# Kernel tuning notes

Measured on AMD Instinct MI355X. Metric: run time of the kernel, lower is better.

The kernel has to match this reference:

```python
import jax, jax.numpy as jnp
import numpy as np

C_IN = 128
C_HID = 128


def setup_inputs() -> dict:
    key = jax.random.key(0)
    ks = jax.random.split(key, 10)
    B, I, J = 1, 384, 384
    x = jax.random.normal(ks[0], (B, I, J, C_IN), dtype=jnp.float32)
    mask = jnp.ones((B, I, J), dtype=jnp.float32)
    # LayerNorm params
    ln_gamma = jnp.ones((C_IN,), jnp.float32)
    ln_beta = jnp.zeros((C_IN,), jnp.float32)
    # Projections (stored as [in, out] for x @ W)
    W_a_p = jax.random.normal(ks[1], (C_IN, C_HID), jnp.float32) * 0.02
    b_a_p = jnp.zeros((C_HID,), jnp.float32)
    W_a_g = jax.random.normal(ks[2], (C_IN, C_HID), jnp.float32) * 0.01
    W_b_p = jax.random.normal(ks[3], (C_IN, C_HID), jnp.float32) * 0.02
    b_b_p = jnp.zeros((C_HID,), jnp.float32)
    W_b_g = jax.random.normal(ks[4], (C_IN, C_HID), jnp.float32) * 0.01
    W_z = jax.random.normal(ks[5], (C_HID, C_IN), jnp.float32) * (0.02 / np.sqrt(C_HID))
    b_z = jnp.zeros((C_IN,), jnp.float32)
    return dict(x=x, mask=mask, ln_gamma=ln_gamma, ln_beta=ln_beta,
                W_a_p=W_a_p, b_a_p=b_a_p, W_a_g=W_a_g,
                W_b_p=W_b_p, b_b_p=b_b_p, W_b_g=W_b_g,
                W_z=W_z, b_z=b_z)


def _layer_norm(x, gamma, beta, eps=1e-5):
    mu = jnp.mean(x, axis=-1, keepdims=True)
    var = jnp.mean(jnp.square(x - mu), axis=-1, keepdims=True)
    return (x - mu) * jax.lax.rsqrt(var + eps) * gamma + beta


def reference(x, mask, ln_gamma, ln_beta, W_a_p, b_a_p, W_a_g, W_b_p, b_b_p, W_b_g, W_z, b_z):
    # x: [B, I, J, C_in], mask: [B, I, J]; outgoing triangle multiplication
    xn = _layer_norm(x, ln_gamma, ln_beta)
    m = mask[..., None]
    a = (xn @ W_a_p + b_a_p) * jax.nn.sigmoid(xn @ W_a_g) * m  # [B,I,J,Ch]
    b = (xn @ W_b_p + b_b_p) * jax.nn.sigmoid(xn @ W_b_g) * m  # [B,I,J,Ch]
    # outgoing: sum over k of a[...,i,k,c] * b[...,k,j,c]
    o = jnp.einsum('bikc,bkjc->bijc', a, b)
    o = o @ W_z + b_z
    return x + o
```

## Files before the change

### kernel.cpp

```cpp
#include <hip/hip_runtime.h>

typedef __bf16 bf16;
typedef bf16 bf16x4 __attribute__((ext_vector_type(4)));
typedef bf16 bf16x8 __attribute__((ext_vector_type(8)));
typedef float f32x4 __attribute__((ext_vector_type(4)));
typedef int ivec4 __attribute__((ext_vector_type(4)));

#define PTOT 147456
#define N384 384

static __device__ __forceinline__ f32x4 mfma16(bf16x8 a, bf16x8 b, f32x4 c) {
  return __builtin_amdgcn_mfma_f32_16x16x32_bf16(a, b, c, 0, 0, 0);
}

static __device__ __forceinline__ void gload_lds16(const bf16* g, bf16* lds) {
  __builtin_amdgcn_global_load_lds(
      (const __attribute__((address_space(1))) void*)g,
      (__attribute__((address_space(3))) void*)lds, 16, 0, 0);
}

__global__ __launch_bounds__(256) void k_prep(
    const float* __restrict__ w0, const float* __restrict__ w1,
    const float* __restrict__ w2, const float* __restrict__ w3,
    const float* __restrict__ w4, bf16* __restrict__ wt)
{
  const int m = blockIdx.x;
  const float* src = (m == 0) ? w0 : (m == 1) ? w1 : (m == 2) ? w2 : (m == 3) ? w3 : w4;
  bf16* dst = wt + m * 16384;
  for (int slot = threadIdx.x; slot < 2048; slot += 256) {
    const int l  = slot & 63;
    const int ks = (slot >> 6) & 3;
    const int n  = slot >> 8;
    const int ch = n * 16 + (l & 15);
    const int kb = ks * 32 + (l >> 4) * 8;
    bf16 tmp[8] __attribute__((aligned(16)));
    #pragma unroll
    for (int e = 0; e < 8; ++e)
      tmp[e] = (bf16)src[(size_t)(kb + e) * 128 + ch];
    *(ivec4*)(dst + slot * 8) = *(const ivec4*)tmp;
  }
}

__global__ __launch_bounds__(256) void k1_ln_proj(
    const float* __restrict__ x, const float* __restrict__ mask,
    const float* __restrict__ gamma, const float* __restrict__ beta,
    const float* __restrict__ bap, const float* __restrict__ bbp,
    const bf16* __restrict__ wt,
    bf16* __restrict__ a_t, bf16* __restrict__ b_t)
{
  __shared__ __align__(16) bf16 xn[64 * 128];
  __shared__ __align__(16) bf16 wl[4 * 2 * 4 * 512];
  __shared__ float ml[64];

  const int t = threadIdx.x;
  const int l = t & 63;
  const int w = t >> 6;
  const int p0 = blockIdx.x << 6;
  const int fr = l & 15, fq = l >> 4;

  const bf16* wsrc = wt + w * 16384 + l * 8;
  bf16* wdst = wl + w * 4096;
  #pragma unroll
  for (int n2 = 0; n2 < 2; ++n2)
    #pragma unroll
    for (int ks = 0; ks < 4; ++ks)
      gload_lds16(wsrc + ((n2 * 4 + ks) << 9), wdst + n2 * 2048 + ks * 512);

  if (t < 64) ml[t] = mask[p0 + t];

  const int csub = (t & 7) << 4;
  f32x4 g4[4], bt4[4];
  #pragma unroll
  for (int i = 0; i < 4; ++i) {
    g4[i]  = *(const f32x4*)(gamma + csub + i * 4);
    bt4[i] = *(const f32x4*)(beta  + csub + i * 4);
  }
  #pragma unroll
  for (int it = 0; it < 2; ++it) {
    const int row = (t >> 3) + it * 32;
    f32x4 v[4];
    const float* xb = x + (size_t)(p0 + row) * 128 + csub;
    #pragma unroll
    for (int i = 0; i < 4; ++i) v[i] = *(const f32x4*)(xb + i * 4);

    float s = 0.f, s2 = 0.f;
    #pragma unroll
    for (int i = 0; i < 4; ++i)
      #pragma unroll
      for (int j = 0; j < 4; ++j) { const float f = v[i][j]; s += f; s2 += f * f; }
    #pragma unroll
    for (int m = 1; m < 8; m <<= 1) {
      s  += __shfl_xor(s, m, 64);
      s2 += __shfl_xor(s2, m, 64);
    }
    const float mu = s * (1.f / 128.f);
    const float rs = rsqrtf(s2 * (1.f / 128.f) - mu * mu + 1e-5f);

    bf16x8 xv0, xv1;
    #pragma unroll
    for (int i = 0; i < 4; ++i)
      #pragma unroll
      for (int j = 0; j < 4; ++j) {
        const float f = (v[i][j] - mu) * rs * g4[i][j] + bt4[i][j];
        const int e = i * 4 + j;
        if (e < 8) xv0[e] = (bf16)f; else xv1[e - 8] = (bf16)f;
      }
    const int sw = (row & 7) << 3;
    *(bf16x8*)&xn[row * 128 + (csub ^ sw)]       = xv0;
    *(bf16x8*)&xn[row * 128 + ((csub + 8) ^ sw)] = xv1;
  }
  __syncthreads();

  const int pair = w >> 1;
  const int prow0 = (w & 1) * 32;
  bf16x8 af[2][4];
  #pragma unroll
  for (int mi = 0; mi < 2; ++mi)
    #pragma unroll
    for (int ks = 0; ks < 4; ++ks) {
      const int row = prow0 + mi * 16 + fr;
      af[mi][ks] = *(const bf16x8*)&xn[row * 128 + (((ks * 32 + fq * 8)) ^ ((fr & 7) << 3))];
    }

  const float* bp = pair ? bbp : bap;
  bf16* dst = pair ? b_t : a_t;
  const bf16* wpl = wl + (pair * 2) * 4096 + l * 8;
  const bf16* wgl = wl + (pair * 2 + 1) * 4096 + l * 8;

  #pragma unroll
  for (int p = 0; p < 4; ++p) {
    #pragma unroll
    for (int n2 = 0; n2 < 2; ++n2) {
      const int ch = (p * 2 + n2) * 16 + fr;
      f32x4 aG0 = (f32x4){0.f, 0.f, 0.f, 0.f};
      f32x4 aG1 = (f32x4){0.f, 0.f, 0.f, 0.f};
      #pragma unroll
      for (int ks = 0; ks < 4; ++ks) {
        const bf16x8 bv = *(const bf16x8*)(wgl + n2 * 2048 + ks * 512);
        aG0 = mfma16(af[0][ks], bv, aG0);
        aG1 = mfma16(af[1][ks], bv, aG1);
      }
      f32x4 aP0 = (f32x4){0.f, 0.f, 0.f, 0.f};
      f32x4 aP1 = (f32x4){0.f, 0.f, 0.f, 0.f};
      #pragma unroll
      for (int ks = 0; ks < 4; ++ks) {
        const bf16x8 bv = *(const bf16x8*)(wpl + n2 * 2048 + ks * 512);
        aP0 = mfma16(af[0][ks], bv, aP0);
        aP1 = mfma16(af[1][ks], bv, aP1);
      }
      const float bias = bp[ch];
      #pragma unroll
      for (int mi = 0; mi < 2; ++mi) {
        const f32x4 aG = mi ? aG1 : aG0;
        const f32x4 aP = mi ? aP1 : aP0;
        const int pb = prow0 + mi * 16 + fq * 4;
        const f32x4 m4 = *(const f32x4*)&ml[pb];
        bf16x4 pk;
        #pragma unroll
        for (int r = 0; r < 4; ++r) {
          const float sg = 1.f / (1.f + __expf(-aG[r]));
          pk[r] = (bf16)((aP[r] + bias) * sg * m4[r]);
        }
        *(bf16x4*)(dst + (size_t)ch * PTOT + p0 + pb) = pk;
      }
    }
    if (p < 3) {
      __syncthreads();
      #pragma unroll
      for (int n2 = 0; n2 < 2; ++n2)
        #pragma unroll
        for (int ks = 0; ks < 4; ++ks)
          gload_lds16(wsrc + ((((p + 1) * 2 + n2) * 4 + ks) << 9),
                      wdst + n2 * 2048 + ks * 512);
      __syncthreads();
    }
  }
}

__global__ __launch_bounds__(256) void k2_tri(
    const bf16* __restrict__ a_t, const bf16* __restrict__ b_t, bf16* __restrict__ o_t)
{
  __shared__ __align__(16) bf16 As[128][40];
  __shared__ __align__(16) bf16 Bt[128][40];
  const int t = threadIdx.x, l = t & 63, w = t >> 6;
  const int fr = l & 15, fq = l >> 4;
  const int ti = blockIdx.x;
  const int c  = blockIdx.y;
  const int i0 = (ti / 3) * 128, j0 = (ti % 3) * 128;
  const bf16* ap = a_t + (size_t)c * PTOT;
  const bf16* bp = b_t + (size_t)c * PTOT;
  const int wm = (w >> 1) * 64, wn = (w & 1) * 64;
  const int arow = t >> 2, aseg = t & 3;
  const int bj = t & 127, bkh = (t >> 7) * 16;

  f32x4 acc[4][4];
  #pragma unroll
  for (int mi = 0; mi < 4; ++mi)
    #pragma unroll
    for (int ni = 0; ni < 4; ++ni) acc[mi][ni] = (f32x4){0.f, 0.f, 0.f, 0.f};

  for (int kt = 0; kt < 12; ++kt) {
    const int k0 = kt * 32;
    __syncthreads();
    #pragma unroll
    for (int rep = 0; rep < 2; ++rep) {
      const int row = arow + rep * 64;
      *(ivec4*)&As[row][aseg * 8] =
          *(const ivec4*)(ap + (size_t)(i0 + row) * N384 + k0 + aseg * 8);
    }
    bf16 rb[16] __attribute__((aligned(16)));
    #pragma unroll
    for (int kk = 0; kk < 16; ++kk)
      rb[kk] = bp[(size_t)(k0 + bkh + kk) * N384 + j0 + bj];
    *(ivec4*)&Bt[bj][bkh]     = *(const ivec4*)&rb[0];
    *(ivec4*)&Bt[bj][bkh + 8] = *(const ivec4*)&rb[8];
    __syncthreads();

    bf16x8 af[4], bfv[4];
    #pragma unroll
    for (int mi = 0; mi < 4; ++mi)
      af[mi] = *(const bf16x8*)&As[wm + mi * 16 + fr][fq * 8];
    #pragma unroll
    for (int ni = 0; ni < 4; ++ni)
      bfv[ni] = *(const bf16x8*)&Bt[wn + ni * 16 + fr][fq * 8];
    #pragma unroll
    for (int mi = 0; mi < 4; ++mi)
      #pragma unroll
      for (int ni = 0; ni < 4; ++ni)
        acc[mi][ni] = mfma16(bfv[ni], af[mi], acc[mi][ni]);
  }

  bf16* op = o_t + (size_t)c * PTOT;
  #pragma unroll
  for (int mi = 0; mi < 4; ++mi) {
    const int irow = i0 + wm + mi * 16 + fr;
    #pragma unroll
    for (int ni = 0; ni < 4; ++ni) {
      const int jcol = j0 + wn + ni * 16 + fq * 4;
      bf16x4 pk;
      #pragma unroll
      for (int r = 0; r < 4; ++r) pk[r] = (bf16)acc[mi][ni][r];
      *(bf16x4*)(op + (size_t)irow * N384 + jcol) = pk;
    }
  }
}

__global__ __launch_bounds__(256) void k3_out(
    const bf16* __restrict__ o_t, const bf16* __restrict__ wtz,
    const float* __restrict__ x, const float* __restrict__ bz,
    float* __restrict__ out)
{
  __shared__ __align__(16) bf16 Ao[64][136];
  const int t = threadIdx.x, l = t & 63, w = t >> 6;
  const int fr = l & 15, fq = l >> 4;
  const int p0 = blockIdx.x << 6;
  const int pos = t & 63, chh = (t >> 6) * 32;

  bf16 rb[32] __attribute__((aligned(16)));
  #pragma unroll
  for (int cc = 0; cc < 32; ++cc)
    rb[cc] = o_t[(size_t)(chh + cc) * PTOT + p0 + pos];
  #pragma unroll
  for (int q = 0; q < 4; ++q)
    *(ivec4*)&Ao[pos][chh + q * 8] = *(const ivec4*)&rb[q * 8];
  __syncthreads();

  bf16x8 af[4];
  #pragma unroll
  for (int ks = 0; ks < 4; ++ks)
    af[ks] = *(const bf16x8*)&Ao[w * 16 + fr][ks * 32 + fq * 8];

  const bf16* wzf = wtz + l * 8;
  f32x4 acc[8];
  #pragma unroll
  for (int n = 0; n < 8; ++n) acc[n] = (f32x4){0.f, 0.f, 0.f, 0.f};
  #pragma unroll
  for (int n = 0; n < 8; ++n)
    #pragma unroll
    for (int ks = 0; ks < 4; ++ks) {
      const bf16x8 bfv = *(const bf16x8*)(wzf + ((n * 4 + ks) << 9));
      acc[n] = mfma16(bfv, af[ks], acc[n]);
    }

  const int pp = p0 + w * 16 + fr;
  #pragma unroll
  for (int n = 0; n < 8; ++n) {
    const int ch = n * 16 + fq * 4;
    const f32x4 b4 = *(const f32x4*)(bz + ch);
    const size_t idx = (size_t)pp * 128 + ch;
    const f32x4 x4 = *(const f32x4*)(x + idx);
    f32x4 o4;
    #pragma unroll
    for (int r = 0; r < 4; ++r) o4[r] = x4[r] + acc[n][r] + b4[r];
    *(f32x4*)(out + idx) = o4;
  }
}

extern "C" void kernel_launch(void* const* d_in, const int* in_sizes, int n_in,
                              void* d_out, int out_size, void* d_ws, size_t ws_size,
                              hipStream_t stream) {
  const float* x     = (const float*)d_in[0];
  const float* mask  = (const float*)d_in[1];
  const float* gamma = (const float*)d_in[2];
  const float* beta  = (const float*)d_in[3];
  const float* Wap   = (const float*)d_in[4];
  const float* bap   = (const float*)d_in[5];
  const float* Wag   = (const float*)d_in[6];
  const float* Wbp   = (const float*)d_in[7];
  const float* bbp   = (const float*)d_in[8];
  const float* Wbg   = (const float*)d_in[9];
  const float* Wz    = (const float*)d_in[10];
  const float* bz    = (const float*)d_in[11];

  char* ws = (char*)d_ws;
  bf16* wt  = (bf16*)ws;
  bf16* a_t = (bf16*)(ws + 163840);
  bf16* b_t = a_t + (size_t)128 * PTOT;
  bf16* o_t = b_t + (size_t)128 * PTOT;
  float* out = (float*)d_out;

  k_prep<<<5, 256, 0, stream>>>(Wap, Wag, Wbp, Wbg, Wz, wt);
  k1_ln_proj<<<2304, 256, 0, stream>>>(x, mask, gamma, beta, bap, bbp, wt, a_t, b_t);
  k2_tri<<<dim3(9, 128), 256, 0, stream>>>(a_t, b_t, o_t);
  k3_out<<<2304, 256, 0, stream>>>(o_t, wt + 4 * 16384, x, bz, out);
}
```

Measured before the change: 140.7 us.

## Double-buffer weight loads in LN-projection kernel with larger 512-thread tiles

The weight layout from k_prep is reorganised so that each 16-channel slice of all four projection matrices is contiguous. k1 now processes 128 rows per block with 8 waves and double-buffers the weight slices in LDS, prefetching the next slice while computing the current one. This replaces the old pattern of two barriers around each synchronous reload. The aim is to hide weight-load latency and halve per-pixel weight traffic, at the cost of more LDS per block (about 64KB), which may lower occupancy.

```diff
diff --git a/kernel.cpp b/kernel.cpp
--- a/kernel.cpp
+++ b/kernel.cpp
@@ -26,7 +26,6 @@
 {
   const int m = blockIdx.x;
   const float* src = (m == 0) ? w0 : (m == 1) ? w1 : (m == 2) ? w2 : (m == 3) ? w3 : w4;
-  bf16* dst = wt + m * 16384;
   for (int slot = threadIdx.x; slot < 2048; slot += 256) {
     const int l  = slot & 63;
     const int ks = (slot >> 6) & 3;
@@ -37,36 +36,38 @@
     #pragma unroll
     for (int e = 0; e < 8; ++e)
       tmp[e] = (bf16)src[(size_t)(kb + e) * 128 + ch];
-    *(ivec4*)(dst + slot * 8) = *(const ivec4*)tmp;
-  }
-}
-
-__global__ __launch_bounds__(256) void k1_ln_proj(
+    bf16* dst = (m < 4)
+        ? wt + (size_t)((n * 16 + m * 4 + ks) * 64 + l) * 8
+        : wt + 4 * 16384 + (size_t)((n * 4 + ks) * 64 + l) * 8;
+    *(ivec4*)dst = *(const ivec4*)tmp;
+  }
+}
+
+__global__ __launch_bounds__(512, 4) void k1_ln_proj(
     const float* __restrict__ x, const float* __restrict__ mask,
     const float* __restrict__ gamma, const float* __restrict__ beta,
     const float* __restrict__ bap, const float* __restrict__ bbp,
     const bf16* __restrict__ wt,
     bf16* __restrict__ a_t, bf16* __restrict__ b_t)
 {
-  __shared__ __align__(16) bf16 xn[64 * 128];
-  __shared__ __align__(16) bf16 wl[4 * 2 * 4 * 512];
-  __shared__ float ml[64];
+  __shared__ __align__(16) bf16 xn[128 * 128];
+  __shared__ __align__(16) bf16 wl[2 * 8192];
+  __shared__ float ml[128];
 
   const int t = threadIdx.x;
   const int l = t & 63;
   const int w = t >> 6;
-  const int p0 = blockIdx.x << 6;
+  const int p0 = blockIdx.x << 7;
   const int fr = l & 15, fq = l >> 4;
-
-  const bf16* wsrc = wt + w * 16384 + l * 8;
-  bf16* wdst = wl + w * 4096;
-  #pragma unroll
-  for (int n2 = 0; n2 < 2; ++n2)
-    #pragma unroll
-    for (int ks = 0; ks < 4; ++ks)
-      gload_lds16(wsrc + ((n2 * 4 + ks) << 9), wdst + n2 * 2048 + ks * 512);
-
-  if (t < 64) ml[t] = mask[p0 + t];
+  const int pair = w & 1;
+  const int prow0 = (w >> 1) * 32;
+
+  const bf16* wsrc = wt + l * 8;
+  const int c0 = w * 2;
+  gload_lds16(wsrc + ((c0) << 9),     wl + c0 * 512);
+  gload_lds16(wsrc + ((c0 + 1) << 9), wl + (c0 + 1) * 512);
+
+  if (t < 128) ml[t] = mask[p0 + t];
 
   const int csub = (t & 7) << 4;
   f32x4 g4[4], bt4[4];
@@ -77,7 +78,7 @@
   }
   #pragma unroll
   for (int it = 0; it < 2; ++it) {
-    const int row = (t >> 3) + it * 32;
+    const int row = (t >> 3) + it * 64;
     f32x4 v[4];
     const float* xb = x + (size_t)(p0 + row) * 128 + csub;
     #pragma unroll
@@ -111,69 +112,65 @@
   }
   __syncthreads();
 
-  const int pair = w >> 1;
-  const int prow0 = (w & 1) * 32;
   bf16x8 af[2][4];
   #pragma unroll
   for (int mi = 0; mi < 2; ++mi)
     #pragma unroll
     for (int ks = 0; ks < 4; ++ks) {
       const int row = prow0 + mi * 16 + fr;
-      af[mi][ks] = *(const bf16x8*)&xn[row * 128 + (((ks * 32 + fq * 8)) ^ ((fr & 7) << 3))];
+      af[mi][ks] = *(const bf16x8*)&xn[row * 128 + ((ks * 32 + fq * 8) ^ ((fr & 7) << 3))];
     }
 
   const float* bp = pair ? bbp : bap;
   bf16* dst = pair ? b_t : a_t;
-  const bf16* wpl = wl + (pair * 2) * 4096 + l * 8;
-  const bf16* wgl = wl + (pair * 2 + 1) * 4096 + l * 8;
-
-  #pragma unroll
-  for (int p = 0; p < 4; ++p) {
-    #pragma unroll
-    for (int n2 = 0; n2 < 2; ++n2) {
-      const int ch = (p * 2 + n2) * 16 + fr;
-      f32x4 aG0 = (f32x4){0.f, 0.f, 0.f, 0.f};
-      f32x4 aG1 = (f32x4){0.f, 0.f, 0.f, 0.f};
-      #pragma unroll
-      for (int ks = 0; ks < 4; ++ks) {
-        const bf16x8 bv = *(const bf16x8*)(wgl + n2 * 2048 + ks * 512);
-        aG0 = mfma16(af[0][ks], bv, aG0);
-        aG1 = mfma16(af[1][ks], bv, aG1);
+  float biasv[8];
+  #pragma unroll
+  for (int p = 0; p < 8; ++p) biasv[p] = bp[p * 16 + fr];
+
+  #pragma unroll
+  for (int p = 0; p < 8; ++p) {
+    if (p < 7) {
+      bf16* nb = wl + ((p + 1) & 1) * 8192;
+      gload_lds16(wsrc + (((p + 1) * 16 + c0) << 9),     nb + c0 * 512);
+      gload_lds16(wsrc + (((p + 1) * 16 + c0 + 1) << 9), nb + (c0 + 1) * 512);
+    }
+    const bf16* buf = wl + (p & 1) * 8192 + l * 8;
+    const bf16* wpl = buf + (pair * 2) * 2048;
+    const bf16* wgl = buf + (pair * 2 + 1) * 2048;
+
+    f32x4 aG0 = (f32x4){0.f, 0.f, 0.f, 0.f};
+    f32x4 aG1 = (f32x4){0.f, 0.f, 0.f, 0.f};
+    #pragma unroll
+    for (int ks = 0; ks < 4; ++ks) {
+      const bf16x8 bv = *(const bf16x8*)(wgl + ks * 512);
+      aG0 = mfma16(af[0][ks], bv, aG0);
+      aG1 = mfma16(af[1][ks], bv, aG1);
+    }
+    f32x4 aP0 = (f32x4){0.f, 0.f, 0.f, 0.f};
+    f32x4 aP1 = (f32x4){0.f, 0.f, 0.f, 0.f};
+    #pragma unroll
+    for (int ks = 0; ks < 4; ++ks) {
+      const bf16x8 bv = *(const bf16x8*)(wpl + ks * 512);
+      aP0 = mfma16(af[0][ks], bv, aP0);
+      aP1 = mfma16(af[1][ks], bv, aP1);
+    }
+    const int ch = p * 16 + fr;
+    const float bias = biasv[p];
+    #pragma unroll
+    for (int mi = 0; mi < 2; ++mi) {
+      const f32x4 aG = mi ? aG1 : aG0;
+      const f32x4 aP = mi ? aP1 : aP0;
+      const int pb = prow0 + mi * 16 + fq * 4;
+      const f32x4 m4 = *(const f32x4*)&ml[pb];
+      bf16x4 pk;
+      #pragma unroll
+      for (int r = 0; r < 4; ++r) {
+        const float sg = 1.f / (1.f + __expf(-aG[r]));
+        pk[r] = (bf16)((aP[r] + bias) * sg * m4[r]);
       }
-      f32x4 aP0 = (f32x4){0.f, 0.f, 0.f, 0.f};
-      f32x4 aP1 = (f32x4){0.f, 0.f, 0.f, 0.f};
-      #pragma unroll
-      for (int ks = 0; ks < 4; ++ks) {
-        const bf16x8 bv = *(const bf16x8*)(wpl + n2 * 2048 + ks * 512);
-        aP0 = mfma16(af[0][ks], bv, aP0);
-        aP1 = mfma16(af[1][ks], bv, aP1);
-      }
-      const float bias = bp[ch];
-      #pragma unroll
-      for (int mi = 0; mi < 2; ++mi) {
-        const f32x4 aG = mi ? aG1 : aG0;
-        const f32x4 aP = mi ? aP1 : aP0;
-        const int pb = prow0 + mi * 16 + fq * 4;
-        const f32x4 m4 = *(const f32x4*)&ml[pb];
-        bf16x4 pk;
-        #pragma unroll
-        for (int r = 0; r < 4; ++r) {
-          const float sg = 1.f / (1.f + __expf(-aG[r]));
-          pk[r] = (bf16)((aP[r] + bias) * sg * m4[r]);
-        }
-        *(bf16x4*)(dst + (size_t)ch * PTOT + p0 + pb) = pk;
-      }
-    }
-    if (p < 3) {
-      __syncthreads();
-      #pragma unroll
-      for (int n2 = 0; n2 < 2; ++n2)
-        #pragma unroll
-        for (int ks = 0; ks < 4; ++ks)
-          gload_lds16(wsrc + ((((p + 1) * 2 + n2) * 4 + ks) << 9),
-                      wdst + n2 * 2048 + ks * 512);
-      __syncthreads();
-    }
+      *(bf16x4*)(dst + (size_t)ch * PTOT + p0 + pb) = pk;
+    }
+    if (p < 7) __syncthreads();
   }
 }
 
@@ -320,7 +317,7 @@
   float* out = (float*)d_out;
 
   k_prep<<<5, 256, 0, stream>>>(Wap, Wag, Wbp, Wbg, Wz, wt);
-  k1_ln_proj<<<2304, 256, 0, stream>>>(x, mask, gamma, beta, bap, bbp, wt, a_t, b_t);
+  k1_ln_proj<<<1152, 512, 0, stream>>>(x, mask, gamma, beta, bap, bbp, wt, a_t, b_t);
   k2_tri<<<dim3(9, 128), 256, 0, stream>>>(a_t, b_t, o_t);
   k3_out<<<2304, 256, 0, stream>>>(o_t, wt + 4 * 16384, x, bz, out);
 }
```

New measurement: 143.9 us (median of 2 runs). 2.3% more time.
